# Optimization experiments

Measured on AMD Instinct MI355X. Metric: run time of the kernel, lower is better.

The kernel has to match this reference:

```python
import jax, jax.numpy as jnp
import numpy as np

DIM = 256
HEADS = 4
HEAD_DIM = DIM // HEADS          # 64
KEY_DIM = HEAD_DIM // 2          # 32 (attn_ratio=0.5)
HIDDEN = DIM + 2 * KEY_DIM * HEADS  # 512
B, H, W = 2, 64, 64
EPS = 1e-5


def _conv2d(x, w, groups=1, pad=0):
    return jax.lax.conv_general_dilated(
        x, w, window_strides=(1, 1), padding=[(pad, pad), (pad, pad)],
        dimension_numbers=('NCHW', 'OIHW', 'NCHW'), feature_group_count=groups)


def _bn(x, g, b, m, v):
    scale = g / jnp.sqrt(v + EPS)
    return x * scale[None, :, None, None] + (b - m * scale)[None, :, None, None]


def setup_inputs() -> dict:
    key = jax.random.key(0)
    ks = jax.random.split(key, 16)
    d = {
        'x': jax.random.normal(ks[0], (B, DIM, H, W), jnp.float32),
        'qkv_w': jax.random.normal(ks[1], (HIDDEN, DIM, 1, 1), jnp.float32) * 0.05,
        'qkv_g': jax.random.uniform(ks[2], (HIDDEN,), jnp.float32, 0.5, 1.5),
        'qkv_b': jax.random.normal(ks[3], (HIDDEN,), jnp.float32) * 0.1,
        'qkv_m': jax.random.normal(ks[4], (HIDDEN,), jnp.float32) * 0.1,
        'qkv_v': jax.random.uniform(ks[5], (HIDDEN,), jnp.float32, 0.5, 1.5),
        'proj_w': jax.random.normal(ks[6], (DIM, DIM, 1, 1), jnp.float32) * 0.05,
        'proj_g': jax.random.uniform(ks[7], (DIM,), jnp.float32, 0.5, 1.5),
        'proj_b': jax.random.normal(ks[8], (DIM,), jnp.float32) * 0.1,
        'proj_m': jax.random.normal(ks[9], (DIM,), jnp.float32) * 0.1,
        'proj_v': jax.random.uniform(ks[10], (DIM,), jnp.float32, 0.5, 1.5),
        'pe_w': jax.random.normal(ks[11], (DIM, 1, 3, 3), jnp.float32) * 0.1,
        'pe_g': jax.random.uniform(ks[12], (DIM,), jnp.float32, 0.5, 1.5),
        'pe_b': jax.random.normal(ks[13], (DIM,), jnp.float32) * 0.1,
        'pe_m': jax.random.normal(ks[14], (DIM,), jnp.float32) * 0.1,
        'pe_v': jax.random.uniform(ks[15], (DIM,), jnp.float32, 0.5, 1.5),
    }
    return d


def reference(x, qkv_w, qkv_g, qkv_b, qkv_m, qkv_v,
              proj_w, proj_g, proj_b, proj_m, proj_v,
              pe_w, pe_g, pe_b, pe_m, pe_v):
    b, c, h, w = x.shape
    n = h * w
    scale = KEY_DIM ** -0.5

    qkv = _bn(_conv2d(x, qkv_w), qkv_g, qkv_b, qkv_m, qkv_v)  # [b, hidden, h, w]
    qkv = qkv.reshape(b, HEADS, 2 * KEY_DIM + HEAD_DIM, n)
    q = qkv[:, :, :KEY_DIM]                       # [b, heads, key_dim, n]
    k = qkv[:, :, KEY_DIM:2 * KEY_DIM]            # [b, heads, key_dim, n]
    v = qkv[:, :, 2 * KEY_DIM:]                   # [b, heads, head_dim, n]

    # attn[b,h,i,j] = sum_d q[b,h,d,i] * k[b,h,d,j] * scale; softmax over j
    attn = jnp.einsum('bhdi,bhdj->bhij', q, k) * scale
    attn = jax.nn.softmax(attn, axis=-1)

    # y = v @ attn^T : out[b,h,d,i] = sum_j v[b,h,d,j] * attn[b,h,i,j]
    y = jnp.einsum('bhdj,bhij->bhdi', v, attn).reshape(b, c, h, w)

    pe = _bn(_conv2d(v.reshape(b, c, h, w), pe_w, groups=c, pad=1),
             pe_g, pe_b, pe_m, pe_v)
    y = y + pe
    return _bn(_conv2d(y, proj_w), proj_g, proj_b, proj_m, proj_v)
```

## Files before the change

### kernel.cpp

```cpp
#include <hip/hip_runtime.h>
#include <hip/hip_bf16.h>

#define NSP 4096
#define BEPS 1e-5f
#define JSPLIT 4
#define JCHUNK (NSP / JSPLIT)

using short8  = __attribute__((ext_vector_type(8))) short;
using f32x4   = __attribute__((ext_vector_type(4))) float;

#define SCALE_LOG2E 0.25500526940103816f

__device__ __forceinline__ float b2f(unsigned short u) {
  return __uint_as_float(((unsigned)u) << 16);
}
__device__ __forceinline__ unsigned short f2b(float x) {
  unsigned u = __float_as_uint(x);
  u += 0x7fffu + ((u >> 16) & 1u);
  return (unsigned short)(u >> 16);
}
__device__ __forceinline__ unsigned pk_bf16(float a, float b) {
  return ((unsigned)f2b(b) << 16) | (unsigned)f2b(a);
}

__global__ __launch_bounds__(256) void cast_w_kernel(
    const float* __restrict__ qkv_w, const float* __restrict__ proj_w,
    unsigned short* __restrict__ wqb, unsigned short* __restrict__ wpb)
{
  const int i = blockIdx.x * 256 + threadIdx.x;
  if (i < 131072)       wqb[i] = f2b(qkv_w[i]);
  else                  wpb[i - 131072] = f2b(proj_w[i - 131072]);
}

__global__ __launch_bounds__(256) void transpose_x_kernel(
    const float* __restrict__ x, unsigned short* __restrict__ xT)
{
  const int n0 = blockIdx.x * 64, c0 = blockIdx.y * 64, b = blockIdx.z;
  __shared__ __align__(16) unsigned short tx[64][72];
  const int t = threadIdx.x;
  const int row = t >> 2;
  const int seg = t & 3;
  {
    const float* xp = x + ((size_t)(b * 256 + c0 + row)) * NSP + n0 + seg * 16;
    #pragma unroll
    for (int q4 = 0; q4 < 4; ++q4) {
      const float4 a = *reinterpret_cast<const float4*>(xp + q4 * 4);
      tx[seg * 16 + q4 * 4 + 0][row] = f2b(a.x);
      tx[seg * 16 + q4 * 4 + 1][row] = f2b(a.y);
      tx[seg * 16 + q4 * 4 + 2][row] = f2b(a.z);
      tx[seg * 16 + q4 * 4 + 3][row] = f2b(a.w);
    }
  }
  __syncthreads();
  const int nrow = t >> 2, ch = t & 3;
  unsigned short* op = xT + ((size_t)(b * NSP + n0 + nrow)) * 256 + c0 + ch * 16;
  *reinterpret_cast<float4*>(op)     = *reinterpret_cast<const float4*>(&tx[nrow][ch * 16]);
  *reinterpret_cast<float4*>(op + 8) = *reinterpret_cast<const float4*>(&tx[nrow][ch * 16 + 8]);
}

__global__ __launch_bounds__(256) void qkv_gemm_kernel(
    const unsigned short* __restrict__ xT, const unsigned short* __restrict__ wqb,
    const float* __restrict__ gg, const float* __restrict__ bb,
    const float* __restrict__ mm, const float* __restrict__ vv,
    unsigned short* __restrict__ qb, unsigned short* __restrict__ kb,
    unsigned short* __restrict__ vb)
{
  const int n0 = blockIdx.x * 64;
  const int cotile = blockIdx.y;
  const int b = blockIdx.z;
  const int co0 = cotile * 64;
  const int t = threadIdx.x;
  __shared__ __align__(16) unsigned short wt[64][136];
  __shared__ __align__(16) unsigned short xt[64][136];
  const int lane = t & 63, wave = t >> 6;
  const int m16 = lane & 15, quad = lane >> 4;
  const int row = t >> 2, seg = t & 3;

  f32x4 acc[4] = {};
  for (int kc = 0; kc < 2; ++kc) {
    if (kc) __syncthreads();
    {
      const unsigned short* wp = wqb + (size_t)(co0 + row) * 256 + kc * 128 + seg * 32;
      const unsigned short* xp = xT + ((size_t)(b * NSP + n0 + row)) * 256 + kc * 128 + seg * 32;
      #pragma unroll
      for (int u = 0; u < 4; ++u) {
        *reinterpret_cast<float4*>(&wt[row][seg * 32 + u * 8]) =
            *reinterpret_cast<const float4*>(wp + u * 8);
        *reinterpret_cast<float4*>(&xt[row][seg * 32 + u * 8]) =
            *reinterpret_cast<const float4*>(xp + u * 8);
      }
    }
    __syncthreads();
    if ((cotile & 1) == 0) {
      #pragma unroll
      for (int ks = 0; ks < 4; ++ks) {
        const short8 af = *reinterpret_cast<const short8*>(&wt[wave * 16 + m16][ks * 32 + quad * 8]);
        #pragma unroll
        for (int nt = 0; nt < 4; ++nt) {
          const short8 bf = *reinterpret_cast<const short8*>(&xt[nt * 16 + m16][ks * 32 + quad * 8]);
          acc[nt] = __builtin_amdgcn_mfma_f32_16x16x32_bf16(af, bf, acc[nt], 0, 0, 0);
        }
      }
    } else {
      #pragma unroll
      for (int ks = 0; ks < 4; ++ks) {
        const short8 bf = *reinterpret_cast<const short8*>(&wt[wave * 16 + m16][ks * 32 + quad * 8]);
        #pragma unroll
        for (int nt = 0; nt < 4; ++nt) {
          const short8 af = *reinterpret_cast<const short8*>(&xt[nt * 16 + m16][ks * 32 + quad * 8]);
          acc[nt] = __builtin_amdgcn_mfma_f32_16x16x32_bf16(af, bf, acc[nt], 0, 0, 0);
        }
      }
    }
  }

  const int head = cotile >> 1;
  const int bh = b * 4 + head;
  if ((cotile & 1) == 0) {
    const int coh = wave * 16 + quad * 4;
    float sc[4], bi[4];
    #pragma unroll
    for (int r = 0; r < 4; ++r) {
      const int c = co0 + coh + r;
      sc[r] = gg[c] * rsqrtf(vv[c] + BEPS);
      bi[r] = bb[c] - mm[c] * sc[r];
    }
    unsigned short* dst = (coh < 32) ? qb : kb;
    const int d0 = coh & 31;
    #pragma unroll
    for (int nt = 0; nt < 4; ++nt) {
      const int i = n0 + nt * 16 + m16;
      uint2 pk2;
      pk2.x = pk_bf16(acc[nt][0] * sc[0] + bi[0], acc[nt][1] * sc[1] + bi[1]);
      pk2.y = pk_bf16(acc[nt][2] * sc[2] + bi[2], acc[nt][3] * sc[3] + bi[3]);
      *reinterpret_cast<uint2*>(dst + ((size_t)bh * NSP + i) * 32 + d0) = pk2;
    }
  } else {
    const int c = co0 + wave * 16 + m16;
    const float sc = gg[c] * rsqrtf(vv[c] + BEPS);
    const float bi = bb[c] - mm[c] * sc;
    const int d = wave * 16 + m16;
    #pragma unroll
    for (int nt = 0; nt < 4; ++nt) {
      const int j = n0 + nt * 16 + quad * 4;
      uint2 pk2;
      pk2.x = pk_bf16(acc[nt][0] * sc + bi, acc[nt][1] * sc + bi);
      pk2.y = pk_bf16(acc[nt][2] * sc + bi, acc[nt][3] * sc + bi);
      *reinterpret_cast<uint2*>(vb + ((size_t)(bh * 64 + d)) * NSP + j) = pk2;
    }
  }
}

__global__ __launch_bounds__(256) void attn_kernel(
    const unsigned short* __restrict__ qb, const unsigned short* __restrict__ kb,
    const unsigned short* __restrict__ vb,
    unsigned short* __restrict__ Opart, float* __restrict__ lpart)
{
  const int i0    = blockIdx.x * 64;
  const int bh    = blockIdx.y;
  const int split = blockIdx.z;
  const int jbase = split * JCHUNK;
  const int t  = threadIdx.x;
  const int lane = t & 63, wave = t >> 6;
  const int m16 = lane & 15, quad = lane >> 4;
  __shared__ __align__(16) short qs[64][40];
  __shared__ __align__(16) short ks[64][40];
  __shared__ __align__(16) short vs[64][72];
  __shared__ __align__(16) short ps[64][72];

  const int srow = t >> 2, schunk = t & 3;
  {
    const unsigned short* qp = qb + ((size_t)bh * NSP + i0) * 32;
    *reinterpret_cast<float4*>(&qs[srow][schunk * 8]) =
        *reinterpret_cast<const float4*>(qp + srow * 32 + schunk * 8);
  }
  __syncthreads();
  const short8 qfrag = *reinterpret_cast<const short8*>(&qs[wave * 16 + m16][quad * 8]);

  float rsum = 0.f;
  f32x4 oacc[4] = {};

  for (int jt0 = 0; jt0 < JCHUNK; jt0 += 64) {
    const int j0 = jbase + jt0;
    __syncthreads();
    {
      const unsigned short* kp = kb + ((size_t)bh * NSP + j0) * 32;
      *reinterpret_cast<float4*>(&ks[srow][schunk * 8]) =
          *reinterpret_cast<const float4*>(kp + srow * 32 + schunk * 8);
      const unsigned short* vp = vb + (size_t)bh * 64 * NSP + j0;
      *reinterpret_cast<float4*>(&vs[srow][schunk * 16]) =
          *reinterpret_cast<const float4*>(vp + (size_t)srow * NSP + schunk * 16);
      *reinterpret_cast<float4*>(&vs[srow][schunk * 16 + 8]) =
          *reinterpret_cast<const float4*>(vp + (size_t)srow * NSP + schunk * 16 + 8);
    }
    __syncthreads();

    f32x4 sacc[4];
    #pragma unroll
    for (int jt = 0; jt < 4; ++jt) {
      const short8 kf = *reinterpret_cast<const short8*>(&ks[jt * 16 + m16][quad * 8]);
      sacc[jt] = __builtin_amdgcn_mfma_f32_16x16x32_bf16(kf, qfrag, (f32x4){0.f,0.f,0.f,0.f}, 0, 0, 0);
    }

    #pragma unroll
    for (int jt = 0; jt < 4; ++jt) {
      float p0 = __builtin_amdgcn_exp2f(sacc[jt][0] * SCALE_LOG2E);
      float p1 = __builtin_amdgcn_exp2f(sacc[jt][1] * SCALE_LOG2E);
      float p2 = __builtin_amdgcn_exp2f(sacc[jt][2] * SCALE_LOG2E);
      float p3 = __builtin_amdgcn_exp2f(sacc[jt][3] * SCALE_LOG2E);
      rsum += (p0 + p1) + (p2 + p3);
      uint2 pk2;
      pk2.x = pk_bf16(p0, p1);
      pk2.y = pk_bf16(p2, p3);
      *reinterpret_cast<uint2*>(&ps[wave * 16 + m16][jt * 16 + quad * 4]) = pk2;
    }

    const short8 pa0 = *reinterpret_cast<const short8*>(&ps[wave * 16 + m16][quad * 8]);
    const short8 pa1 = *reinterpret_cast<const short8*>(&ps[wave * 16 + m16][32 + quad * 8]);
    #pragma unroll
    for (int dt = 0; dt < 4; ++dt) {
      const short8 v0 = *reinterpret_cast<const short8*>(&vs[dt * 16 + m16][quad * 8]);
      const short8 v1 = *reinterpret_cast<const short8*>(&vs[dt * 16 + m16][32 + quad * 8]);
      oacc[dt] = __builtin_amdgcn_mfma_f32_16x16x32_bf16(pa0, v0, oacc[dt], 0, 0, 0);
      oacc[dt] = __builtin_amdgcn_mfma_f32_16x16x32_bf16(pa1, v1, oacc[dt], 0, 0, 0);
    }
  }

  rsum += __shfl_xor(rsum, 16);
  rsum += __shfl_xor(rsum, 32);
  if (quad == 0)
    lpart[((size_t)split * 8 + bh) * NSP + i0 + wave * 16 + m16] = rsum;

  #pragma unroll
  for (int dt = 0; dt < 4; ++dt) {
    const int d = dt * 16 + m16;
    uint2 pk2;
    pk2.x = pk_bf16(oacc[dt][0], oacc[dt][1]);
    pk2.y = pk_bf16(oacc[dt][2], oacc[dt][3]);
    *reinterpret_cast<uint2*>(Opart +
        (((size_t)split * 8 + bh) * 64 + d) * NSP + i0 + wave * 16 + quad * 4) = pk2;
  }
}

__global__ __launch_bounds__(256) void fuse_kernel(
    const unsigned short* __restrict__ Opart, const float* __restrict__ lpart,
    const unsigned short* __restrict__ vb,
    const float* __restrict__ pw, const float* __restrict__ pg,
    const float* __restrict__ pb, const float* __restrict__ pm,
    const float* __restrict__ pv,
    unsigned short* __restrict__ yT)
{
  const int py = blockIdx.x;
  const int bh = blockIdx.y;
  const int b = bh >> 2, h = bh & 3;
  const int t = threadIdx.x;
  const int d = t >> 2, seg = t & 3;
  __shared__ float lsum[64];
  __shared__ __align__(16) unsigned short yt[64][72];

  if (t < 64) {
    float ls = 0.f;
    #pragma unroll
    for (int s = 0; s < JSPLIT; ++s)
      ls += lpart[((size_t)s * 8 + bh) * NSP + py * 64 + t];
    lsum[t] = ls;
  }
  __syncthreads();

  const int c = h * 64 + d;
  const int i0 = py * 64 + seg * 16;
  float os[16] = {};
  #pragma unroll
  for (int s = 0; s < JSPLIT; ++s) {
    const unsigned short* op = Opart + (((size_t)s * 8 + bh) * 64 + d) * NSP + i0;
    #pragma unroll
    for (int u = 0; u < 16; ++u) os[u] += b2f(op[u]);
  }

  float w9[9];
  #pragma unroll
  for (int i = 0; i < 9; ++i) w9[i] = pw[c * 9 + i];
  const float sc = pg[c] * rsqrtf(pv[c] + BEPS);
  const float bi = pb[c] - pm[c] * sc;
  const unsigned short* vrow = vb + ((size_t)(bh * 64 + d)) * NSP;

  float conv[16] = {};
  #pragma unroll
  for (int dy = -1; dy <= 1; ++dy) {
    const int yy = py + dy;
    if (yy < 0 || yy > 63) continue;
    float vals[18];
    #pragma unroll
    for (int u = 0; u < 18; ++u) {
      const int px = seg * 16 - 1 + u;
      vals[u] = (px >= 0 && px < 64) ? b2f(vrow[yy * 64 + px]) : 0.f;
    }
    const float wr0 = w9[(dy + 1) * 3 + 0], wr1 = w9[(dy + 1) * 3 + 1], wr2 = w9[(dy + 1) * 3 + 2];
    #pragma unroll
    for (int u = 0; u < 16; ++u)
      conv[u] += vals[u] * wr0 + vals[u + 1] * wr1 + vals[u + 2] * wr2;
  }

  #pragma unroll
  for (int u = 0; u < 16; ++u) {
    const float yv = os[u] / lsum[seg * 16 + u] + conv[u] * sc + bi;
    yt[seg * 16 + u][d] = f2b(yv);
  }
  __syncthreads();

  const int prow = t >> 2, ch = t & 3;
  unsigned short* op = yT + ((size_t)(b * NSP + py * 64 + prow)) * 256 + h * 64 + ch * 16;
  *reinterpret_cast<float4*>(op)     = *reinterpret_cast<const float4*>(&yt[prow][ch * 16]);
  *reinterpret_cast<float4*>(op + 8) = *reinterpret_cast<const float4*>(&yt[prow][ch * 16 + 8]);
}

__global__ __launch_bounds__(256) void proj_gemm_kernel(
    const unsigned short* __restrict__ yT, const unsigned short* __restrict__ wpb,
    const float* __restrict__ gg, const float* __restrict__ bb,
    const float* __restrict__ mm, const float* __restrict__ vv,
    float* __restrict__ out)
{
  const int n0 = blockIdx.x * 64;
  const int co0 = blockIdx.y * 64;
  const int b = blockIdx.z;
  const int t = threadIdx.x;
  __shared__ __align__(16) unsigned short wt[64][136];
  __shared__ __align__(16) unsigned short yt[64][136];
  const int lane = t & 63, wave = t >> 6;
  const int m16 = lane & 15, quad = lane >> 4;
  const int row = t >> 2, seg = t & 3;

  f32x4 acc[4] = {};
  for (int kc = 0; kc < 2; ++kc) {
    if (kc) __syncthreads();
    {
      const unsigned short* wp = wpb + (size_t)(co0 + row) * 256 + kc * 128 + seg * 32;
      const unsigned short* yp = yT + ((size_t)(b * NSP + n0 + row)) * 256 + kc * 128 + seg * 32;
      #pragma unroll
      for (int u = 0; u < 4; ++u) {
        *reinterpret_cast<float4*>(&wt[row][seg * 32 + u * 8]) =
            *reinterpret_cast<const float4*>(wp + u * 8);
        *reinterpret_cast<float4*>(&yt[row][seg * 32 + u * 8]) =
            *reinterpret_cast<const float4*>(yp + u * 8);
      }
    }
    __syncthreads();
    #pragma unroll
    for (int ks = 0; ks < 4; ++ks) {
      const short8 bf = *reinterpret_cast<const short8*>(&wt[wave * 16 + m16][ks * 32 + quad * 8]);
      #pragma unroll
      for (int nt = 0; nt < 4; ++nt) {
        const short8 af = *reinterpret_cast<const short8*>(&yt[nt * 16 + m16][ks * 32 + quad * 8]);
        acc[nt] = __builtin_amdgcn_mfma_f32_16x16x32_bf16(af, bf, acc[nt], 0, 0, 0);
      }
    }
  }

  const int c = co0 + wave * 16 + m16;
  const float sc = gg[c] * rsqrtf(vv[c] + BEPS);
  const float bi = bb[c] - mm[c] * sc;
  #pragma unroll
  for (int nt = 0; nt < 4; ++nt) {
    const int n = n0 + nt * 16 + quad * 4;
    float4 ov;
    ov.x = acc[nt][0] * sc + bi; ov.y = acc[nt][1] * sc + bi;
    ov.z = acc[nt][2] * sc + bi; ov.w = acc[nt][3] * sc + bi;
    *reinterpret_cast<float4*>(out + ((size_t)(b * 256 + c)) * NSP + n) = ov;
  }
}

extern "C" void kernel_launch(void* const* d_in, const int* in_sizes, int n_in,
                              void* d_out, int out_size, void* d_ws, size_t ws_size,
                              hipStream_t stream)
{
  const float* x      = (const float*)d_in[0];
  const float* qkv_w  = (const float*)d_in[1];
  const float* qkv_g  = (const float*)d_in[2];
  const float* qkv_b  = (const float*)d_in[3];
  const float* qkv_m  = (const float*)d_in[4];
  const float* qkv_v  = (const float*)d_in[5];
  const float* proj_w = (const float*)d_in[6];
  const float* proj_g = (const float*)d_in[7];
  const float* proj_b = (const float*)d_in[8];
  const float* proj_m = (const float*)d_in[9];
  const float* proj_v = (const float*)d_in[10];
  const float* pe_w   = (const float*)d_in[11];
  const float* pe_g   = (const float*)d_in[12];
  const float* pe_b   = (const float*)d_in[13];
  const float* pe_m   = (const float*)d_in[14];
  const float* pe_v   = (const float*)d_in[15];
  float* out = (float*)d_out;

  unsigned short* qb = (unsigned short*)d_ws;
  unsigned short* kb = qb + (size_t)8 * NSP * 32;
  unsigned short* vb = kb + (size_t)8 * NSP * 32;
  unsigned short* Opart = vb + (size_t)8 * 64 * NSP;
  float* lpart = (float*)(Opart + (size_t)JSPLIT * 8 * 64 * NSP);
  unsigned short* xT = (unsigned short*)(lpart + (size_t)JSPLIT * 8 * NSP);
  unsigned short* yT = xT + (size_t)2 * NSP * 256;
  unsigned short* wqb = yT + (size_t)2 * NSP * 256;
  unsigned short* wpb = wqb + (size_t)512 * 256;

  cast_w_kernel<<<dim3(768), 256, 0, stream>>>(qkv_w, proj_w, wqb, wpb);
  transpose_x_kernel<<<dim3(64, 4, 2), 256, 0, stream>>>(x, xT);
  qkv_gemm_kernel<<<dim3(64, 8, 2), 256, 0, stream>>>(xT, wqb, qkv_g, qkv_b, qkv_m, qkv_v,
                                                      qb, kb, vb);
  attn_kernel<<<dim3(64, 8, JSPLIT), 256, 0, stream>>>(qb, kb, vb, Opart, lpart);
  fuse_kernel<<<dim3(64, 8), 256, 0, stream>>>(Opart, lpart, vb,
                                               pe_w, pe_g, pe_b, pe_m, pe_v, yT);
  proj_gemm_kernel<<<dim3(64, 4, 2), 256, 0, stream>>>(yT, wpb, proj_g, proj_b, proj_m, proj_v,
                                                       out);
}
```

Baseline: 177.4 us.

## Double query rows per attention block to reuse K/V tiles across more rows

Each attention block now handles 128 query rows instead of 64, with each wave computing two 16-row query fragments against the same K and V tiles loaded into shared memory. This halves the number of K/V global loads and LDS staging passes per query row, and the K fragments are read once and reused for both row groups. The grid in the i dimension is halved to 32 blocks, and launch bounds request 3 blocks per CU. The cost is more registers and LDS per block and fewer blocks overall (1024), which may reduce occupancy and latency hiding.

```diff
diff --git a/kernel.cpp b/kernel.cpp
--- a/kernel.cpp
+++ b/kernel.cpp
@@ -151,35 +151,40 @@
   }
 }
 
-__global__ __launch_bounds__(256) void attn_kernel(
+__global__ __launch_bounds__(256, 3) void attn_kernel(
     const unsigned short* __restrict__ qb, const unsigned short* __restrict__ kb,
     const unsigned short* __restrict__ vb,
     unsigned short* __restrict__ Opart, float* __restrict__ lpart)
 {
-  const int i0    = blockIdx.x * 64;
+  const int i0    = blockIdx.x * 128;
   const int bh    = blockIdx.y;
   const int split = blockIdx.z;
   const int jbase = split * JCHUNK;
   const int t  = threadIdx.x;
   const int lane = t & 63, wave = t >> 6;
   const int m16 = lane & 15, quad = lane >> 4;
-  __shared__ __align__(16) short qs[64][40];
+  __shared__ __align__(16) short qs[128][40];
   __shared__ __align__(16) short ks[64][40];
   __shared__ __align__(16) short vs[64][72];
-  __shared__ __align__(16) short ps[64][72];
-
-  const int srow = t >> 2, schunk = t & 3;
+  __shared__ __align__(16) short ps[128][72];
+
   {
     const unsigned short* qp = qb + ((size_t)bh * NSP + i0) * 32;
-    *reinterpret_cast<float4*>(&qs[srow][schunk * 8]) =
-        *reinterpret_cast<const float4*>(qp + srow * 32 + schunk * 8);
+    const int r = t >> 1, h = t & 1;
+    *reinterpret_cast<float4*>(&qs[r][h * 16]) =
+        *reinterpret_cast<const float4*>(qp + r * 32 + h * 16);
+    *reinterpret_cast<float4*>(&qs[r][h * 16 + 8]) =
+        *reinterpret_cast<const float4*>(qp + r * 32 + h * 16 + 8);
   }
   __syncthreads();
-  const short8 qfrag = *reinterpret_cast<const short8*>(&qs[wave * 16 + m16][quad * 8]);
-
-  float rsum = 0.f;
-  f32x4 oacc[4] = {};
-
+  short8 qfrag[2];
+  qfrag[0] = *reinterpret_cast<const short8*>(&qs[wave * 32 + m16][quad * 8]);
+  qfrag[1] = *reinterpret_cast<const short8*>(&qs[wave * 32 + 16 + m16][quad * 8]);
+
+  float rsum[2] = {0.f, 0.f};
+  f32x4 oacc[2][4] = {};
+
+  const int srow = t >> 2, schunk = t & 3;
   for (int jt0 = 0; jt0 < JCHUNK; jt0 += 64) {
     const int j0 = jbase + jt0;
     __syncthreads();
@@ -195,51 +200,71 @@
     }
     __syncthreads();
 
-    f32x4 sacc[4];
-    #pragma unroll
-    for (int jt = 0; jt < 4; ++jt) {
-      const short8 kf = *reinterpret_cast<const short8*>(&ks[jt * 16 + m16][quad * 8]);
-      sacc[jt] = __builtin_amdgcn_mfma_f32_16x16x32_bf16(kf, qfrag, (f32x4){0.f,0.f,0.f,0.f}, 0, 0, 0);
-    }
-
-    #pragma unroll
-    for (int jt = 0; jt < 4; ++jt) {
-      float p0 = __builtin_amdgcn_exp2f(sacc[jt][0] * SCALE_LOG2E);
-      float p1 = __builtin_amdgcn_exp2f(sacc[jt][1] * SCALE_LOG2E);
-      float p2 = __builtin_amdgcn_exp2f(sacc[jt][2] * SCALE_LOG2E);
-      float p3 = __builtin_amdgcn_exp2f(sacc[jt][3] * SCALE_LOG2E);
-      rsum += (p0 + p1) + (p2 + p3);
-      uint2 pk2;
-      pk2.x = pk_bf16(p0, p1);
-      pk2.y = pk_bf16(p2, p3);
-      *reinterpret_cast<uint2*>(&ps[wave * 16 + m16][jt * 16 + quad * 4]) = pk2;
-    }
-
-    const short8 pa0 = *reinterpret_cast<const short8*>(&ps[wave * 16 + m16][quad * 8]);
-    const short8 pa1 = *reinterpret_cast<const short8*>(&ps[wave * 16 + m16][32 + quad * 8]);
+    short8 kf[4];
+    #pragma unroll
+    for (int jt = 0; jt < 4; ++jt)
+      kf[jt] = *reinterpret_cast<const short8*>(&ks[jt * 16 + m16][quad * 8]);
+
+    #pragma unroll
+    for (int it = 0; it < 2; ++it) {
+      f32x4 sacc[4];
+      #pragma unroll
+      for (int jt = 0; jt < 4; ++jt)
+        sacc[jt] = __builtin_amdgcn_mfma_f32_16x16x32_bf16(kf[jt], qfrag[it],
+                                                           (f32x4){0.f,0.f,0.f,0.f}, 0, 0, 0);
+      const int irow = wave * 32 + it * 16 + m16;
+      #pragma unroll
+      for (int jt = 0; jt < 4; ++jt) {
+        float p0 = __builtin_amdgcn_exp2f(sacc[jt][0] * SCALE_LOG2E);
+        float p1 = __builtin_amdgcn_exp2f(sacc[jt][1] * SCALE_LOG2E);
+        float p2 = __builtin_amdgcn_exp2f(sacc[jt][2] * SCALE_LOG2E);
+        float p3 = __builtin_amdgcn_exp2f(sacc[jt][3] * SCALE_LOG2E);
+        rsum[it] += (p0 + p1) + (p2 + p3);
+        uint2 pk2;
+        pk2.x = pk_bf16(p0, p1);
+        pk2.y = pk_bf16(p2, p3);
+        *reinterpret_cast<uint2*>(&ps[irow][jt * 16 + quad * 4]) = pk2;
+      }
+    }
+
+    short8 pa[2][2];
+    #pragma unroll
+    for (int it = 0; it < 2; ++it) {
+      pa[it][0] = *reinterpret_cast<const short8*>(&ps[wave * 32 + it * 16 + m16][quad * 8]);
+      pa[it][1] = *reinterpret_cast<const short8*>(&ps[wave * 32 + it * 16 + m16][32 + quad * 8]);
+    }
     #pragma unroll
     for (int dt = 0; dt < 4; ++dt) {
       const short8 v0 = *reinterpret_cast<const short8*>(&vs[dt * 16 + m16][quad * 8]);
       const short8 v1 = *reinterpret_cast<const short8*>(&vs[dt * 16 + m16][32 + quad * 8]);
-      oacc[dt] = __builtin_amdgcn_mfma_f32_16x16x32_bf16(pa0, v0, oacc[dt], 0, 0, 0);
-      oacc[dt] = __builtin_amdgcn_mfma_f32_16x16x32_bf16(pa1, v1, oacc[dt], 0, 0, 0);
-    }
-  }
-
-  rsum += __shfl_xor(rsum, 16);
-  rsum += __shfl_xor(rsum, 32);
-  if (quad == 0)
-    lpart[((size_t)split * 8 + bh) * NSP + i0 + wave * 16 + m16] = rsum;
-
-  #pragma unroll
-  for (int dt = 0; dt < 4; ++dt) {
-    const int d = dt * 16 + m16;
-    uint2 pk2;
-    pk2.x = pk_bf16(oacc[dt][0], oacc[dt][1]);
-    pk2.y = pk_bf16(oacc[dt][2], oacc[dt][3]);
-    *reinterpret_cast<uint2*>(Opart +
-        (((size_t)split * 8 + bh) * 64 + d) * NSP + i0 + wave * 16 + quad * 4) = pk2;
-  }
+      #pragma unroll
+      for (int it = 0; it < 2; ++it) {
+        oacc[it][dt] = __builtin_amdgcn_mfma_f32_16x16x32_bf16(pa[it][0], v0, oacc[it][dt], 0, 0, 0);
+        oacc[it][dt] = __builtin_amdgcn_mfma_f32_16x16x32_bf16(pa[it][1], v1, oacc[it][dt], 0, 0, 0);
+      }
+    }
+  }
+
+  #pragma unroll
+  for (int it = 0; it < 2; ++it) {
+    float rs = rsum[it];
+    rs += __shfl_xor(rs, 16);
+    rs += __shfl_xor(rs, 32);
+    if (quad == 0)
+      lpart[((size_t)split * 8 + bh) * NSP + i0 + wave * 32 + it * 16 + m16] = rs;
+  }
+
+  #pragma unroll
+  for (int it = 0; it < 2; ++it)
+    #pragma unroll
+    for (int dt = 0; dt < 4; ++dt) {
+      const int d = dt * 16 + m16;
+      uint2 pk2;
+      pk2.x = pk_bf16(oacc[it][dt][0], oacc[it][dt][1]);
+      pk2.y = pk_bf16(oacc[it][dt][2], oacc[it][dt][3]);
+      *reinterpret_cast<uint2*>(Opart +
+          (((size_t)split * 8 + bh) * 64 + d) * NSP + i0 + wave * 32 + it * 16 + quad * 4) = pk2;
+    }
 }
 
 __global__ __launch_bounds__(256) void fuse_kernel(
@@ -405,7 +430,7 @@
   transpose_x_kernel<<<dim3(64, 4, 2), 256, 0, stream>>>(x, xT);
   qkv_gemm_kernel<<<dim3(64, 8, 2), 256, 0, stream>>>(xT, wqb, qkv_g, qkv_b, qkv_m, qkv_v,
                                                       qb, kb, vb);
-  attn_kernel<<<dim3(64, 8, JSPLIT), 256, 0, stream>>>(qb, kb, vb, Opart, lpart);
+  attn_kernel<<<dim3(32, 8, JSPLIT), 256, 0, stream>>>(qb, kb, vb, Opart, lpart);
   fuse_kernel<<<dim3(64, 8), 256, 0, stream>>>(Opart, lpart, vb,
                                                pe_w, pe_g, pe_b, pe_m, pe_v, yT);
   proj_gemm_kernel<<<dim3(64, 4, 2), 256, 0, stream>>>(yT, wpb, proj_g, proj_b, proj_m, proj_v,
```

Measured after the change: 169.9 us. 1.04x faster.
